# Performance work log

Measured on AMD Instinct MI355X. Metric: run time of the kernel, lower is better.

Reference implementation:

```python
import jax, jax.numpy as jnp
import numpy as np

PAD = 1
THRESH = 10.0


def setup_inputs() -> dict:
    key = jax.random.key(0)
    k1, k2, k3 = jax.random.split(key, 3)
    x = jax.random.normal(k1, (8, 16, 62, 62), dtype=jnp.float32)
    W = jax.random.normal(k2, (32, 16, 3, 3), dtype=jnp.float32)
    b = jax.random.normal(k3, (32,), dtype=jnp.float32)
    return {"x": x, "W": W, "b": b}


def reference(x, W, b):
    # ZeroPad2d(padding) on all four sides
    x = jnp.pad(x, ((0, 0), (0, 0), (PAD, PAD), (PAD, PAD)))
    T, C, xr, xc = x.shape
    O, _, wr, wc = W.shape
    L = xr * xc

    # get_xfft_thresh: 1D FFT over flattened HxW, zero coeffs with |Re| < thresh
    xf = jnp.fft.fft(x.reshape(T, C, L))                      # (T,C,L) complex
    xf = jnp.where(jnp.abs(xf.real) < THRESH, jnp.zeros_like(xf), xf)

    # get_Wfft: zero-pad kernel to (xr,xc) bottom/right, flatten, reverse along
    # length (flipud(flip([0,1])) nets to a flip of the last axis only), then FFT
    Wp = jnp.pad(W, ((0, 0), (0, 0), (0, xr - wr), (0, xc - wc))).reshape(O, C, L)
    Wf = jnp.fft.fft(Wp[:, :, ::-1])                          # (O,C,L) complex

    # fftConv1D, batched over (image, out_channel):
    y = jnp.fft.ifft(xf[:, None, :, :] * Wf[None, :, :, :]).real  # (T,O,C,L)
    # torch.roll(y, 1) with no dims rolls the FLATTENED (C*L) tensor by 1
    y = jnp.roll(y.reshape(T, O, C * L), 1, axis=-1).reshape(T, O, C, xr, xc)
    y = y.sum(axis=2)                                         # sum over in-channels
    ans_r, ans_c = xr - wr + 1, xc - wc + 1
    y = y[:, :, :ans_r, :ans_c]
    return y + b[None, :, None, None]
```

## Files before the change

### kernel.cpp

```cpp
#include <hip/hip_runtime.h>
#include <math.h>

#define TWO_PI 6.28318530717958647692f
#define NT     1024
#define RPW    4
#define PITCH  65
#define THRESH 10.0f
#define C128   0.998795456205172393f
#define S128   0.049067674327418015f

typedef float v2f __attribute__((ext_vector_type(2)));

__device__ __forceinline__ int brev6(int x) {
    return (int)(__brev((unsigned)x) >> 26);
}

__device__ __forceinline__ v2f cmul_add(v2f a, v2f b, v2f acc) {
    acc += (v2f){a.x, a.x} * b;
    acc += (v2f){a.y, a.y} * (v2f){-b.y, b.x};
    return acc;
}

struct Tw6 { v2f t[6]; };

__device__ __forceinline__ Tw6 make_tw6(int lane, float sign) {
    Tw6 T;
    #pragma unroll
    for (int s = 0; s < 6; ++s) {
        int h = 1 << s;
        int j = lane & (h - 1);
        float ang = sign * (TWO_PI / 64.0f) * (float)(j * (32 >> s));
        float c, si;
        __sincosf(ang, &si, &c);
        T.t[s] = (v2f){c, si};
    }
    return T;
}

template<int R>
__device__ __forceinline__ void fft64_dif_t(float (&re)[R], float (&im)[R],
                                            int lane, const Tw6& T) {
    #pragma unroll
    for (int s = 5; s >= 0; --s) {
        const int h = 1 << s;
        float wr = T.t[s].x, wi = T.t[s].y;
        bool upper = (lane & h) != 0;
        float cwr = upper ? wr : 1.0f;
        float cwi = upper ? wi : 0.0f;
        float sgn = upper ? -1.0f : 1.0f;
        #pragma unroll
        for (int m = 0; m < R; ++m) {
            float orr = __shfl_xor(re[m], h, 64);
            float oii = __shfl_xor(im[m], h, 64);
            float ar = fmaf(sgn, re[m], orr);
            float ai = fmaf(sgn, im[m], oii);
            re[m] = ar * cwr - ai * cwi;
            im[m] = ar * cwi + ai * cwr;
        }
    }
}

template<int R>
__device__ __forceinline__ void fft64_dit_t(float (&re)[R], float (&im)[R],
                                            int lane, const Tw6& T) {
    #pragma unroll
    for (int s = 0; s < 6; ++s) {
        const int h = 1 << s;
        float wr = T.t[s].x, wi = T.t[s].y;
        bool upper = (lane & h) != 0;
        float cwr = upper ? wr : 1.0f;
        float cwi = upper ? wi : 0.0f;
        float sgn = upper ? -1.0f : 1.0f;
        #pragma unroll
        for (int m = 0; m < R; ++m) {
            float tr = re[m] * cwr - im[m] * cwi;
            float ti = re[m] * cwi + im[m] * cwr;
            float orr = __shfl_xor(tr, h, 64);
            float oii = __shfl_xor(ti, h, 64);
            re[m] = fmaf(sgn, tr, orr);
            im[m] = fmaf(sgn, ti, oii);
        }
    }
}

__device__ __forceinline__ v2f tap_combine(const v2f (&T)[9], v2f u, v2f v,
                                           v2f v2) {
    v2f g0 = cmul_add(v2, T[2], cmul_add(v, T[1], T[0]));
    v2f g1 = cmul_add(v2, T[5], cmul_add(v, T[4], T[3]));
    v2f g2 = cmul_add(v2, T[8], cmul_add(v, T[7], T[6]));
    return cmul_add(u, cmul_add(u, g2, g1), g0);
}

__global__ __launch_bounds__(NT) void fwd_kernel(const float* __restrict__ x,
                                                 float2* __restrict__ X) {
    __shared__ float sre[64 * PITCH];
    __shared__ float sim[64 * PITCH];
    const int bId  = blockIdx.x;
    const int t    = bId & 7;
    const int rr_  = bId >> 3;
    const int c    = rr_ & 15;
    const int h    = rr_ >> 4;
    const int task = t * 16 + c;
    const int tid  = threadIdx.x;
    const int lane = tid & 63;
    const int w    = tid >> 6;
    const float* xr = x + (size_t)task * 62 * 62;

    for (int idx = tid; idx < 4096; idx += NT) {
        int r = idx >> 6, s = idx & 63;
        float v = 0.0f;
        if (r >= 1 && r <= 62 && s >= 1 && s <= 62)
            v = xr[(r - 1) * 62 + (s - 1)];
        sre[r * PITCH + s] = v;
    }
    __syncthreads();

    const Tw6 Tf = make_tw6(lane, -1.0f);

    float re[RPW], im[RPW];
    #pragma unroll
    for (int m = 0; m < RPW; ++m) {
        re[m] = sre[lane * PITCH + (w * RPW + m)];
        im[m] = 0.0f;
    }
    fft64_dif_t<RPW>(re, im, lane, Tf);
    const int k1 = brev6(lane);
    #pragma unroll
    for (int m = 0; m < RPW; ++m) {
        int n2 = w * RPW + m;
        float cr, ci;
        __sincosf(-(TWO_PI / 4096.0f) * (float)(k1 * n2), &ci, &cr);
        float rv = re[m] * cr - im[m] * ci;
        im[m]    = re[m] * ci + im[m] * cr;
        re[m]    = rv;
    }
    __syncthreads();
    #pragma unroll
    for (int m = 0; m < RPW; ++m) {
        int n2 = w * RPW + m;
        sre[k1 * PITCH + n2] = re[m];
        sim[k1 * PITCH + n2] = im[m];
    }
    __syncthreads();

    float rb[2], ib[2];
    const int row0 = 16 * h + w;
    rb[0] = sre[row0 * PITCH + lane];
    ib[0] = sim[row0 * PITCH + lane];
    rb[1] = sre[32 * PITCH + lane];
    ib[1] = sim[32 * PITCH + lane];
    fft64_dif_t<2>(rb, ib, lane, Tf);
    float2* Xrow = X + (size_t)task * 4096;
    {
        float rv = rb[0], iv = ib[0];
        if (fabsf(rv) < THRESH) { rv = 0.0f; iv = 0.0f; }
        Xrow[row0 * 64 + lane] = make_float2(rv, iv);
    }
    if (h == 1 && w == 0) {
        float rv = rb[1], iv = ib[1];
        if (fabsf(rv) < THRESH) { rv = 0.0f; iv = 0.0f; }
        Xrow[32 * 64 + lane] = make_float2(rv, iv);
    }
}

__global__ __launch_bounds__(NT, 3) void conv_kernel(const float2* __restrict__ X,
                                                     const float* __restrict__ W,
                                                     const float* __restrict__ b,
                                                     float* __restrict__ out) {
    __shared__ float sre[64 * PITCH];
    __shared__ float sim[64 * PITCH];
    const int t    = blockIdx.x & 7;
    const int o    = blockIdx.x >> 3;
    const int tid  = threadIdx.x;
    const int lane = tid & 63;
    const int w    = tid >> 6;

    const int k2 = brev6(lane);
    float elr, eli;
    __sincosf((TWO_PI / 64.0f) * (float)k2, &eli, &elr);

    const Tw6 Ti = make_tw6(lane, +1.0f);

    const int rA = 2 * w, rB = 2 * w + 1;
    float uAr, uAi, vAr, vAi, uBr, uBi, vBr, vBi;
    __sincosf((TWO_PI / 64.0f) * (float)rA, &uAi, &uAr);
    __sincosf((TWO_PI / 4096.0f) * (float)rA, &vAi, &vAr);
    __sincosf((TWO_PI / 64.0f) * (float)rB, &uBi, &uBr);
    __sincosf((TWO_PI / 4096.0f) * (float)rB, &vBi, &vBr);
    v2f uA = {uAr, uAi};
    v2f vA = {vAr * elr - vAi * eli, vAr * eli + vAi * elr};
    v2f v2A = {vA.x * vA.x - vA.y * vA.y, 2.0f * vA.x * vA.y};
    v2f uB = {uBr, uBi};
    v2f vB = {vBr * elr - vBi * eli, vBr * eli + vBi * elr};
    v2f v2B = {vB.x * vB.x - vB.y * vB.y, 2.0f * vB.x * vB.y};

    const float2* Xt = X + (size_t)t * 16 * 4096 + lane;
    const float*  wo = W + o * 144;

    v2f xA[16], xB[16];
    #pragma unroll
    for (int c = 0; c < 16; ++c) {
        { float2 q = Xt[c * 4096 + rA * 64]; xA[c] = (v2f){q.x, q.y}; }
        { float2 q = Xt[c * 4096 + rB * 64]; xB[c] = (v2f){q.x, q.y}; }
    }
    v2f TA[9], TB[9];
    #pragma unroll
    for (int q = 0; q < 9; ++q) { TA[q] = (v2f){0,0}; TB[q] = (v2f){0,0}; }
    #pragma unroll
    for (int c = 0; c < 16; ++c) {
        const float* wc = wo + c * 9;
        #pragma unroll
        for (int q = 0; q < 9; ++q) {
            float wq = wc[q];
            TA[q] += xA[c] * wq;
            TB[q] += xB[c] * wq;
        }
    }
    v2f SA = tap_combine(TA, uA, vA, v2A);
    v2f SB = tap_combine(TB, uB, vB, v2B);

    sre[rA * PITCH + k2] = SA.x; sim[rA * PITCH + k2] = SA.y;
    sre[rB * PITCH + k2] = SB.x; sim[rB * PITCH + k2] = SB.y;

    if (w == 0) {
        v2f xC[16];
        #pragma unroll
        for (int c = 0; c < 16; ++c) {
            float2 q = Xt[c * 4096 + 32 * 64]; xC[c] = (v2f){q.x, q.y};
        }
        v2f TC[9];
        #pragma unroll
        for (int q = 0; q < 9; ++q) TC[q] = (v2f){0,0};
        #pragma unroll
        for (int c = 0; c < 16; ++c) {
            const float* wc = wo + c * 9;
            #pragma unroll
            for (int q = 0; q < 9; ++q) TC[q] += xC[c] * wc[q];
        }
        v2f vC = {C128 * elr - S128 * eli, C128 * eli + S128 * elr};
        v2f v2C = {vC.x * vC.x - vC.y * vC.y, 2.0f * vC.x * vC.y};
        v2f g0 = cmul_add(v2C, TC[2], cmul_add(vC, TC[1], TC[0]));
        v2f g1 = cmul_add(v2C, TC[5], cmul_add(vC, TC[4], TC[3]));
        v2f g2 = cmul_add(v2C, TC[8], cmul_add(vC, TC[7], TC[6]));
        v2f SC = g0 - g1 + g2;
        sre[32 * PITCH + k2] = SC.x; sim[32 * PITCH + k2] = SC.y;
    }
    __syncthreads();

    float re[RPW], im[RPW];
    #pragma unroll
    for (int m = 0; m < RPW; ++m) {
        int k1 = w * RPW + m;
        if (k1 <= 32) {
            re[m] = sre[k1 * PITCH + k2];
            im[m] = sim[k1 * PITCH + k2];
        } else {
            int k1p = 64 - k1, k2p = 63 - k2;
            re[m] =  sre[k1p * PITCH + k2p];
            im[m] = -sim[k1p * PITCH + k2p];
        }
    }
    __syncthreads();

    fft64_dit_t<RPW>(re, im, lane, Ti);
    #pragma unroll
    for (int m = 0; m < RPW; ++m) {
        int k1 = w * RPW + m;
        float cr, ci;
        __sincosf((TWO_PI / 4096.0f) * (float)(lane * k1), &ci, &cr);
        float rv = re[m] * cr - im[m] * ci;
        im[m]    = re[m] * ci + im[m] * cr;
        re[m]    = rv;
    }
    #pragma unroll
    for (int m = 0; m < RPW; ++m) {
        int k1 = w * RPW + m;
        sre[k1 * PITCH + lane] = re[m];
        sim[k1 * PITCH + lane] = im[m];
    }
    __syncthreads();
    #pragma unroll
    for (int m = 0; m < RPW; ++m) {
        int n2 = w * RPW + m;
        re[m] = sre[lane * PITCH + n2];
        im[m] = sim[lane * PITCH + n2];
    }
    fft64_dif_t<RPW>(re, im, lane, Ti);
    __syncthreads();
    const int n1 = brev6(lane);
    #pragma unroll
    for (int m = 0; m < RPW; ++m) {
        int n2 = w * RPW + m;
        sre[n1 * PITCH + n2] = re[m];
    }
    __syncthreads();
    const float bias = b[o];
    float* orow = out + (size_t)(t * 32 + o) * 62 * 62;
    for (int idx = tid; idx < 62 * 62; idx += NT) {
        int r = idx / 62, s = idx - r * 62;
        orow[idx] = sre[r * PITCH + s] * (1.0f / 4096.0f) + bias;
    }
}

extern "C" void kernel_launch(void* const* d_in, const int* in_sizes, int n_in,
                              void* d_out, int out_size, void* d_ws, size_t ws_size,
                              hipStream_t stream) {
    const float* x = (const float*)d_in[0];
    const float* W = (const float*)d_in[1];
    const float* b = (const float*)d_in[2];
    float* out = (float*)d_out;
    float2* X = (float2*)d_ws;

    fwd_kernel<<<dim3(256), dim3(NT), 0, stream>>>(x, X);
    conv_kernel<<<dim3(256), dim3(NT), 0, stream>>>(X, W, b, out);
}
```

Measured before the change: 76.18 us.

## Run first-pass FFT only on unique Hermitian rows and mirror results

The first inverse FFT pass is now applied directly to the 33 unique spectrum rows in registers, and Hermitian symmetry is used to write the conjugate rows into shared memory. This removes one shared-memory round trip, one barrier, and roughly half the first-pass FFT work. The trade-off is extra mirrored stores and the reliance on the symmetry mapping being exactly right, since the k2 index reversal is now folded into the transform output.

```diff
diff --git a/kernel.cpp b/kernel.cpp
--- a/kernel.cpp
+++ b/kernel.cpp
@@ -219,9 +219,32 @@
     v2f SA = tap_combine(TA, uA, vA, v2A);
     v2f SB = tap_combine(TB, uB, vB, v2B);
 
-    sre[rA * PITCH + k2] = SA.x; sim[rA * PITCH + k2] = SA.y;
-    sre[rB * PITCH + k2] = SB.x; sim[rB * PITCH + k2] = SB.y;
-
+    float pr[2] = {SA.x, SB.x};
+    float pi[2] = {SA.y, SB.y};
+    fft64_dit_t<2>(pr, pi, lane, Ti);
+
+    {
+        float cr, ci;
+        __sincosf((TWO_PI / 4096.0f) * (float)(lane * rA), &ci, &cr);
+        float rv = pr[0] * cr - pi[0] * ci;
+        pi[0]    = pr[0] * ci + pi[0] * cr;
+        pr[0]    = rv;
+        __sincosf((TWO_PI / 4096.0f) * (float)(lane * rB), &ci, &cr);
+        rv    = pr[1] * cr - pi[1] * ci;
+        pi[1] = pr[1] * ci + pi[1] * cr;
+        pr[1] = rv;
+    }
+
+    sre[rA * PITCH + lane] = pr[0]; sim[rA * PITCH + lane] = pi[0];
+    sre[rB * PITCH + lane] = pr[1]; sim[rB * PITCH + lane] = pi[1];
+    {
+        sre[(64 - rB) * PITCH + lane] =  pr[1];
+        sim[(64 - rB) * PITCH + lane] = -pi[1];
+    }
+    if (w > 0) {
+        sre[(64 - rA) * PITCH + lane] =  pr[0];
+        sim[(64 - rA) * PITCH + lane] = -pi[0];
+    }
     if (w == 0) {
         v2f xC[16];
         #pragma unroll
@@ -243,42 +266,18 @@
         v2f g1 = cmul_add(v2C, TC[5], cmul_add(vC, TC[4], TC[3]));
         v2f g2 = cmul_add(v2C, TC[8], cmul_add(vC, TC[7], TC[6]));
         v2f SC = g0 - g1 + g2;
-        sre[32 * PITCH + k2] = SC.x; sim[32 * PITCH + k2] = SC.y;
+        float cr_[1] = {SC.x}, ci_[1] = {SC.y};
+        fft64_dit_t<1>(cr_, ci_, lane, Ti);
+        float cr, ci;
+        __sincosf((TWO_PI / 128.0f) * (float)lane, &ci, &cr);
+        float rv = cr_[0] * cr - ci_[0] * ci;
+        float iv = cr_[0] * ci + ci_[0] * cr;
+        sre[32 * PITCH + lane] = rv;
+        sim[32 * PITCH + lane] = iv;
     }
     __syncthreads();
 
     float re[RPW], im[RPW];
-    #pragma unroll
-    for (int m = 0; m < RPW; ++m) {
-        int k1 = w * RPW + m;
-        if (k1 <= 32) {
-            re[m] = sre[k1 * PITCH + k2];
-            im[m] = sim[k1 * PITCH + k2];
-        } else {
-            int k1p = 64 - k1, k2p = 63 - k2;
-            re[m] =  sre[k1p * PITCH + k2p];
-            im[m] = -sim[k1p * PITCH + k2p];
-        }
-    }
-    __syncthreads();
-
-    fft64_dit_t<RPW>(re, im, lane, Ti);
-    #pragma unroll
-    for (int m = 0; m < RPW; ++m) {
-        int k1 = w * RPW + m;
-        float cr, ci;
-        __sincosf((TWO_PI / 4096.0f) * (float)(lane * k1), &ci, &cr);
-        float rv = re[m] * cr - im[m] * ci;
-        im[m]    = re[m] * ci + im[m] * cr;
-        re[m]    = rv;
-    }
-    #pragma unroll
-    for (int m = 0; m < RPW; ++m) {
-        int k1 = w * RPW + m;
-        sre[k1 * PITCH + lane] = re[m];
-        sim[k1 * PITCH + lane] = im[m];
-    }
-    __syncthreads();
     #pragma unroll
     for (int m = 0; m < RPW; ++m) {
         int n2 = w * RPW + m;
```

After: 74.13 us. -2.7%, faster.
